# Optimization experiments

Measured on AMD Instinct MI355X. Metric: run time of the kernel, lower is better.

The kernel has to match this reference:

```python
import jax, jax.numpy as jnp
import numpy as np

NEG_INF = -1e9

def setup_inputs() -> dict:
    key = jax.random.key(0)
    ks = jax.random.split(key, 7)
    B, NQ, NK, DQ, DK, DV, DH = 16, 128, 2048, 256, 256, 128, 64
    queries = jax.random.normal(ks[0], (B, NQ, DQ), dtype=jnp.float32)
    keys = jax.random.normal(ks[1], (B, NK, DK), dtype=jnp.float32)
    values = jax.random.normal(ks[2], (B, NK, DV), dtype=jnp.float32)
    valid_lens = jax.random.randint(ks[3], (B,), 1, NK + 1, dtype=jnp.int32)
    Wq = jax.random.normal(ks[4], (DQ, DH), dtype=jnp.float32) / np.sqrt(DQ)
    Wk = jax.random.normal(ks[5], (DK, DH), dtype=jnp.float32) / np.sqrt(DK)
    wv = jax.random.normal(ks[6], (DH,), dtype=jnp.float32) / np.sqrt(DH)
    return {"queries": queries, "keys": keys, "values": values,
            "valid_lens": valid_lens, "Wq": Wq, "Wk": Wk, "wv": wv}


def reference(queries, keys, values, valid_lens, Wq, Wk, wv):
    # Additive (Bahdanau) attention.
    q = jnp.einsum('bqd,dh->bqh', queries, Wq)   # [B, nq, dH]
    k = jnp.einsum('bkd,dh->bkh', keys, Wk)      # [B, nk, dH]
    # broadcast add -> tanh -> reduce with wv: scores [B, nq, nk]
    feat = jnp.tanh(q[:, :, None, :] + k[:, None, :, :])  # [B, nq, nk, dH]
    scores = jnp.einsum('bqkh,h->bqk', feat, wv)
    # masked softmax over nk using per-batch valid lengths
    nk = keys.shape[1]
    mask = jnp.arange(nk)[None, None, :] < valid_lens[:, None, None]  # [B,1,nk]
    scores = jnp.where(mask, scores, NEG_INF)
    attn = jax.nn.softmax(scores, axis=-1)
    # dropout is identity at eval time
    return jnp.einsum('bqk,bkv->bqv', attn, values)  # [B, nq, dv]
```

## Files before the change

### kernel.cpp

```cpp
#include <hip/hip_runtime.h>
#include <stddef.h>


__device__ __forceinline__ float fast_rcp(float x)  { return __builtin_amdgcn_rcpf(x); }
__device__ __forceinline__ float fast_exp2(float x) { return __builtin_amdgcn_exp2f(x); }

#define C2F 2.88539008177792681f
#define L2E 1.44269504088896340f

template<int MODE>
__device__ __forceinline__
void proj_body(const float* __restrict__ inb, const float* __restrict__ W,
               float* __restrict__ out, int b, int r0, int rowsPerB, int t)
{
  __shared__ float4 Wlds[256 * 16];
  __shared__ float  klds[64 * 36];

  const float4* W4 = (const float4*)W;
  #pragma unroll
  for (int i = 0; i < 16; ++i) Wlds[t + 256 * i] = W4[t + 256 * i];

  const int j = t >> 4;
  const int g = t & 15;

  float acc[4][4];
  #pragma unroll
  for (int m = 0; m < 4; ++m)
    acc[m][0] = acc[m][1] = acc[m][2] = acc[m][3] = 0.f;

  for (int dc = 0; dc < 8; ++dc) {
    {
      const int row = t >> 2, cs = (t & 3) * 8;
      const float* s = inb + row * 256 + dc * 32 + cs;
      float4 a0 = *(const float4*)s;
      float4 a1 = *(const float4*)(s + 4);
      float* dst = &klds[row * 36 + cs];
      *(float4*)dst       = a0;
      *(float4*)(dst + 4) = a1;
    }
    __syncthreads();
    #pragma unroll
    for (int d = 0; d < 32; ++d) {
      float4 w4 = Wlds[(dc * 32 + d) * 16 + j];
      #pragma unroll
      for (int m = 0; m < 4; ++m) {
        float kv = klds[(g + 16 * m) * 36 + d];
        acc[m][0] = fmaf(kv, w4.x, acc[m][0]);
        acc[m][1] = fmaf(kv, w4.y, acc[m][1]);
        acc[m][2] = fmaf(kv, w4.z, acc[m][2]);
        acc[m][3] = fmaf(kv, w4.w, acc[m][3]);
      }
    }
    __syncthreads();
  }

  if constexpr (MODE == 1) {
    #pragma unroll
    for (int m = 0; m < 4; ++m) {
      int k = r0 + g + 16 * m;
      size_t base = ((size_t)(b * 16 + (k >> 7)) * 64) * 128 + (k & 127);
      #pragma unroll
      for (int i = 0; i < 4; ++i)
        out[base + (size_t)(4 * j + i) * 128] = fast_exp2(C2F * acc[m][i]);
    }
  } else if constexpr (MODE == 2) {
    #pragma unroll
    for (int m = 0; m < 4; ++m) {
      int k = r0 + g + 16 * m;
      size_t base = (size_t)(b * 16 + (k >> 7)) * 8192 + (size_t)(k & 127) * 2;
      float e0 = fast_exp2(C2F * acc[m][0]);
      float e1 = fast_exp2(C2F * acc[m][1]);
      float e2 = fast_exp2(C2F * acc[m][2]);
      float e3 = fast_exp2(C2F * acc[m][3]);
      *(float2*)&out[base + (size_t)(2 * j) * 256]     = make_float2(e0, e1);
      *(float2*)&out[base + (size_t)(2 * j + 1) * 256] = make_float2(e2, e3);
    }
  } else {
    #pragma unroll
    for (int m = 0; m < 4; ++m) {
      int row = r0 + g + 16 * m;
      float4 o;
      o.x = fast_exp2(C2F * acc[m][0]);
      o.y = fast_exp2(C2F * acc[m][1]);
      o.z = fast_exp2(C2F * acc[m][2]);
      o.w = fast_exp2(C2F * acc[m][3]);
      *(float4*)&out[((size_t)b * rowsPerB + row) * 64 + 4 * j] = o;
    }
  }
}

__global__ __launch_bounds__(256)
void proj_qk_kernel(const float* __restrict__ queries, const float* __restrict__ keys,
                    const float* __restrict__ Wq, const float* __restrict__ Wk,
                    float* __restrict__ Eq, float* __restrict__ EkP,
                    const int* __restrict__ vlens)
{
  const int blk = blockIdx.x;
  if (blk >= 512) {
    const int idx = blk - 512;
    const int b = idx & 15, rt = idx >> 4, r0 = rt * 64;
    proj_body<0>(queries + ((size_t)b * 128 + r0) * 256, Wq, Eq, b, r0, 128,
                 threadIdx.x);
  } else {
    const int b = blk & 15, rt = blk >> 4, r0 = rt * 64;
    if (r0 >= vlens[b]) return;
    proj_body<2>(keys + ((size_t)b * 2048 + r0) * 256, Wk, EkP, b, r0, 2048,
                 threadIdx.x);
  }
}

template<int MODE, bool CHECK>
__global__ __launch_bounds__(256)
void proj_kernel(const float* __restrict__ in, const float* __restrict__ W,
                 float* __restrict__ out, const int* __restrict__ vlens,
                 int rowsPerB)
{
  const int t  = threadIdx.x;
  const int b  = blockIdx.x & 15;
  const int rt = blockIdx.x >> 4;
  const int r0 = rt * 64;
  if constexpr (CHECK) {
    if (r0 >= vlens[b]) return;
  }
  proj_body<MODE>(in + ((size_t)b * rowsPerB + r0) * 256, W, out, b, r0,
                  rowsPerB, t);
}

__global__ __launch_bounds__(512, 6)
void scorepv_kernel(const float* __restrict__ Eq, const float* __restrict__ EkP,
                    const float* __restrict__ values, const int* __restrict__ vlens,
                    const float* __restrict__ wv,
                    float* __restrict__ partial, float* __restrict__ tsum)
{
  const int blk = blockIdx.x;
  const int g   = blk >> 3;
  const int qq  = blk & 7;
  const int kt  = g >> 4;
  const int b   = g & 15;
  const int vl  = vlens[b];
  if (kt * 128 >= vl) return;

  __shared__ float ek_lds[64 * 128];

  const int t = threadIdx.x;

  {
    const float4* src = (const float4*)(EkP + (size_t)(b * 16 + kt) * 8192);
    float4* dst = (float4*)ek_lds;
    #pragma unroll
    for (int i = 0; i < 4; ++i) dst[t + 512 * i] = src[t + 512 * i];
  }

  float w0 = 0.f, W1 = 0.f;
  #pragma unroll
  for (int u = 0; u < 16; ++u) {
    float4 v = ((const float4*)wv)[u];
    w0 += v.x + v.y + v.z + v.w;
    W1 += fabsf(v.x) + fabsf(v.y) + fabsf(v.z) + fabsf(v.w);
  }

  __syncthreads();

  const int wave_u = __builtin_amdgcn_readfirstlane(t >> 6);
  const int lane   = t & 63;
  const int q0g    = qq * 16 + wave_u * 2;
  const int kp     = lane * 2;
  const float* eqb = Eq + (size_t)(b * 128 + q0g) * 64;

  float s[2][2] = {{w0, w0}, {w0, w0}};

  const float4* ek4 = (const float4*)ek_lds;
  #pragma unroll 8
  for (int hp = 0; hp < 32; ++hp) {
    float4 e = ek4[hp * 64 + lane];
    float2 wvp = *(const float2*)&wv[2 * hp];
    float wa = -2.0f * wvp.x, wb = -2.0f * wvp.y;
    #pragma unroll
    for (int q = 0; q < 2; ++q) {
      float2 eqp = *(const float2*)&eqb[q * 64 + 2 * hp];
      { float x0 = fmaf(eqp.x, e.x, 1.f), x1 = fmaf(eqp.y, e.y, 1.f);
        float y = fast_rcp(x0 * x1);
        float a = wb * x0; a = fmaf(wa, x1, a);
        s[q][0] = fmaf(a, y, s[q][0]); }
      { float x0 = fmaf(eqp.x, e.z, 1.f), x1 = fmaf(eqp.y, e.w, 1.f);
        float y = fast_rcp(x0 * x1);
        float a = wb * x0; a = fmaf(wa, x1, a);
        s[q][1] = fmaf(a, y, s[q][1]); }
    }
  }

  const int kbase = kt * 128 + kp;
  float p[2][2];
  #pragma unroll
  for (int q = 0; q < 2; ++q) {
    p[q][0] = (kbase     < vl) ? fast_exp2((s[q][0] - W1) * L2E) : 0.f;
    p[q][1] = (kbase + 1 < vl) ? fast_exp2((s[q][1] - W1) * L2E) : 0.f;
  }

  #pragma unroll
  for (int q = 0; q < 2; ++q) {
    float e = p[q][0] + p[q][1];
    #pragma unroll
    for (int m = 1; m < 64; m <<= 1) e += __shfl_xor(e, m, 64);
    if (lane == 0) tsum[(size_t)(b * 16 + kt) * 128 + q0g + q] = e;
  }

  __syncthreads();
  float* p_lds = ek_lds;
  const int q0l = wave_u * 2;
  *(float2*)&p_lds[kp * 20 + q0l]       = make_float2(p[0][0], p[1][0]);
  *(float2*)&p_lds[(kp + 1) * 20 + q0l] = make_float2(p[0][1], p[1][1]);
  __syncthreads();

  const int kg = t >> 7, v = t & 127;
  const int kloc = min(128, vl - kt * 128);
  const int k0 = kg * 32, k1 = min(k0 + 32, kloc);
  const int len = (k1 > k0) ? (k1 - k0) : 0;
  const int nfull = len & ~7;
  const float* vb = values + ((size_t)(b * 2048 + kt * 128)) * 128 + v;
  float acc[16];
  #pragma unroll
  for (int i = 0; i < 16; ++i) acc[i] = 0.f;

  for (int kb = k0; kb < k0 + nfull; kb += 8) {
    float vv[8];
    #pragma unroll
    for (int j = 0; j < 8; ++j) vv[j] = vb[(size_t)(kb + j) * 128];
    #pragma unroll
    for (int j = 0; j < 8; ++j) {
      const float* pr = &p_lds[(kb + j) * 20];
      float4 p0 = *(const float4*)&pr[0];
      float4 p1 = *(const float4*)&pr[4];
      float4 p2 = *(const float4*)&pr[8];
      float4 p3 = *(const float4*)&pr[12];
      float vx = vv[j];
      acc[ 0]=fmaf(p0.x,vx,acc[ 0]); acc[ 1]=fmaf(p0.y,vx,acc[ 1]);
      acc[ 2]=fmaf(p0.z,vx,acc[ 2]); acc[ 3]=fmaf(p0.w,vx,acc[ 3]);
      acc[ 4]=fmaf(p1.x,vx,acc[ 4]); acc[ 5]=fmaf(p1.y,vx,acc[ 5]);
      acc[ 6]=fmaf(p1.z,vx,acc[ 6]); acc[ 7]=fmaf(p1.w,vx,acc[ 7]);
      acc[ 8]=fmaf(p2.x,vx,acc[ 8]); acc[ 9]=fmaf(p2.y,vx,acc[ 9]);
      acc[10]=fmaf(p2.z,vx,acc[10]); acc[11]=fmaf(p2.w,vx,acc[11]);
      acc[12]=fmaf(p3.x,vx,acc[12]); acc[13]=fmaf(p3.y,vx,acc[13]);
      acc[14]=fmaf(p3.z,vx,acc[14]); acc[15]=fmaf(p3.w,vx,acc[15]);
    }
  }
  for (int k = k0 + nfull; k < k1; ++k) {
    float vx = vb[(size_t)k * 128];
    const float* pr = &p_lds[k * 20];
    #pragma unroll
    for (int q = 0; q < 16; ++q) acc[q] = fmaf(pr[q], vx, acc[q]);
  }

  __syncthreads();
  float* red = ek_lds;
  if (kg > 0) {
    #pragma unroll
    for (int q = 0; q < 16; ++q) red[(kg - 1) * 2048 + q * 128 + v] = acc[q];
  }
  __syncthreads();
  if (kg == 0) {
    #pragma unroll
    for (int q = 0; q < 16; ++q) {
      float tot = acc[q] + red[q * 128 + v] + red[2048 + q * 128 + v]
                + red[4096 + q * 128 + v];
      partial[(((size_t)(b * 128 + qq * 16 + q)) * 16 + kt) * 128 + v] = tot;
    }
  }
}

__global__ __launch_bounds__(256)
void reduce_kernel(const float* __restrict__ partial, const float* __restrict__ tsum,
                   const int* __restrict__ vlens, float* __restrict__ out)
{
  const int blk = blockIdx.x;
  const int b   = blk >> 6;
  const int q   = (blk & 63) * 2 + (threadIdx.x >> 7);
  const int v   = threadIdx.x & 127;
  const int ntk = (vlens[b] + 127) >> 7;

  float tot = 0.f;
  for (int i = 0; i < ntk; ++i)
    tot += tsum[(size_t)(b * 16 + i) * 128 + q];

  float acc = 0.f;
  const float* pp = partial + ((size_t)(b * 128 + q)) * 16 * 128 + v;
  for (int i = 0; i < ntk; ++i)
    acc += pp[(size_t)i * 128];

  out[((size_t)(b * 128 + q)) * 128 + v] = acc / tot;
}

__global__ __launch_bounds__(256)
void attn_kernel(const float* __restrict__ Eq, const float* __restrict__ EkT,
                 const float* __restrict__ values, const int* __restrict__ vlens,
                 const float* __restrict__ wv, float* __restrict__ out)
{
  const int t    = threadIdx.x;
  const int b    = blockIdx.x & 15;
  const int qt   = blockIdx.x >> 4;
  const int wave = t >> 6;
  const int lane = t & 63;

  __shared__ float4 sc4[512 * 4];
  __shared__ float  pvp[128 * 5];
  __shared__ float  linvs[4];

  const int vl = vlens[b];

  float eqv[64], wv2[64];
  float w0 = 0.f;
  {
    const float4* eq4 = (const float4*)(Eq + (size_t)(b * 128 + qt * 4 + wave) * 64);
    const float4* wv4 = (const float4*)wv;
    #pragma unroll
    for (int u = 0; u < 16; ++u) {
      float4 e = eq4[u], v = wv4[u];
      eqv[4*u+0] = e.x; eqv[4*u+1] = e.y; eqv[4*u+2] = e.z; eqv[4*u+3] = e.w;
      wv2[4*u+0] = -2.f * v.x; wv2[4*u+1] = -2.f * v.y;
      wv2[4*u+2] = -2.f * v.z; wv2[4*u+3] = -2.f * v.w;
      w0 += v.x + v.y + v.z + v.w;
    }
  }

  const int ktiles = (vl + 127) >> 7;
  const int kp = 2 * lane;
  for (int kt = 0; kt < ktiles; ++kt) {
    const float* tb = EkT + ((size_t)(b * 16 + kt) * 64) * 128 + kp;
    float s0 = w0, s1 = w0;
    #pragma unroll
    for (int h = 0; h < 64; ++h) {
      float2 ek = *(const float2*)(tb + (size_t)h * 128);
      float r0 = fast_rcp(fmaf(eqv[h], ek.x, 1.0f));
      float r1 = fast_rcp(fmaf(eqv[h], ek.y, 1.0f));
      s0 = fmaf(wv2[h], r0, s0);
      s1 = fmaf(wv2[h], r1, s1);
    }
    int k = kt * 128 + kp;
    if (k     >= vl) s0 = -1e9f;
    if (k + 1 >= vl) s1 = -1e9f;
    float* scf = (float*)sc4;
    *(float2*)(scf + (((k >> 2) * 4 + wave) * 4 + (k & 3))) = make_float2(s0, s1);
  }

  const int nq4 = (vl + 3) >> 2;
  float mx = -3e38f;
  for (int Q = lane; Q < nq4; Q += 64) {
    float4 f = sc4[Q * 4 + wave];
    mx = fmaxf(mx, fmaxf(fmaxf(f.x, f.y), fmaxf(f.z, f.w)));
  }
  #pragma unroll
  for (int msk = 1; msk < 64; msk <<= 1) mx = fmaxf(mx, __shfl_xor(mx, msk, 64));
  float lsum = 0.f;
  for (int Q = lane; Q < nq4; Q += 64) {
    float4 f = sc4[Q * 4 + wave];
    f.x = fast_exp2((f.x - mx) * L2E);
    f.y = fast_exp2((f.y - mx) * L2E);
    f.z = fast_exp2((f.z - mx) * L2E);
    f.w = fast_exp2((f.w - mx) * L2E);
    sc4[Q * 4 + wave] = f;
    lsum += f.x + f.y + f.z + f.w;
  }
  #pragma unroll
  for (int msk = 1; msk < 64; msk <<= 1) lsum += __shfl_xor(lsum, msk, 64);
  if (lane == 0) linvs[wave] = fast_rcp(lsum);
  __syncthreads();

  const int grp = t >> 7, v = t & 127;
  float acc[4] = {0.f, 0.f, 0.f, 0.f};
  const float* vb = values + (size_t)b * 2048 * 128 + v;
  for (int Q = grp; Q < nq4; Q += 2) {
    float4 p0 = sc4[Q * 4 + 0], p1 = sc4[Q * 4 + 1];
    float4 p2 = sc4[Q * 4 + 2], p3 = sc4[Q * 4 + 3];
    const float* vk = vb + (size_t)(Q * 4) * 128;
    float x;
    x = vk[0];
    acc[0]=fmaf(p0.x,x,acc[0]); acc[1]=fmaf(p1.x,x,acc[1]);
    acc[2]=fmaf(p2.x,x,acc[2]); acc[3]=fmaf(p3.x,x,acc[3]);
    x = vk[128];
    acc[0]=fmaf(p0.y,x,acc[0]); acc[1]=fmaf(p1.y,x,acc[1]);
    acc[2]=fmaf(p2.y,x,acc[2]); acc[3]=fmaf(p3.y,x,acc[3]);
    x = vk[256];
    acc[0]=fmaf(p0.z,x,acc[0]); acc[1]=fmaf(p1.z,x,acc[1]);
    acc[2]=fmaf(p2.z,x,acc[2]); acc[3]=fmaf(p3.z,x,acc[3]);
    x = vk[384];
    acc[0]=fmaf(p0.w,x,acc[0]); acc[1]=fmaf(p1.w,x,acc[1]);
    acc[2]=fmaf(p2.w,x,acc[2]); acc[3]=fmaf(p3.w,x,acc[3]);
  }
  if (grp == 1) {
    #pragma unroll
    for (int qq = 0; qq < 4; ++qq) pvp[v * 5 + qq] = acc[qq];
  }
  __syncthreads();
  if (grp == 0) {
    #pragma unroll
    for (int qq = 0; qq < 4; ++qq) {
      float tot = acc[qq] + pvp[v * 5 + qq];
      out[((size_t)(b * 128) + qt * 4 + qq) * 128 + v] = tot * linvs[qq];
    }
  }
}

extern "C" void kernel_launch(void* const* d_in, const int* in_sizes, int n_in,
                              void* d_out, int out_size, void* d_ws, size_t ws_size,
                              hipStream_t stream) {
  const float* queries = (const float*)d_in[0];
  const float* keys    = (const float*)d_in[1];
  const float* values  = (const float*)d_in[2];
  const int*   vlens   = (const int*)d_in[3];
  const float* Wq      = (const float*)d_in[4];
  const float* Wk      = (const float*)d_in[5];
  const float* wv      = (const float*)d_in[6];
  float* outp = (float*)d_out;

  float* base    = (float*)d_ws;
  float* Eq      = base;
  float* EkP     = base + 131072;
  float* tsumb   = base + 2228224;
  float* partial = base + 2260992;
  const size_t need = (size_t)(2260992 + 4194304) * 4;

  if (ws_size >= need) {
    hipLaunchKernelGGL(proj_qk_kernel, dim3(544), dim3(256), 0, stream,
                       queries, keys, Wq, Wk, Eq, EkP, vlens);
    hipLaunchKernelGGL(scorepv_kernel, dim3(2048), dim3(512), 0, stream,
                       Eq, EkP, values, vlens, wv, partial, tsumb);
    hipLaunchKernelGGL(reduce_kernel, dim3(1024), dim3(256), 0, stream,
                       partial, tsumb, vlens, outp);
  } else {
    hipLaunchKernelGGL((proj_kernel<0, false>), dim3(32), dim3(256), 0, stream,
                       queries, Wq, Eq, (const int*)nullptr, 128);
    hipLaunchKernelGGL((proj_kernel<1, true>), dim3(512), dim3(256), 0, stream,
                       keys, Wk, EkP, vlens, 2048);
    hipLaunchKernelGGL(attn_kernel, dim3(512), dim3(256), 0, stream,
                       Eq, EkP, values, vlens, wv, outp);
  }
}
```

Baseline: 91.24 us.

## Make score-PV kernel persistent with atomic work queue over 64-key tiles

The score/PV kernel becomes persistent: a fixed grid of 768 blocks pulls work units from a global atomic counter. A small init kernel builds a prefix table over valid 64-key tiles per batch, so only live tiles are scheduled and no blocks launch just to exit early. Key tiles shrink from 128 to 64, with each lane handling one key and two queries. Query and wv values are broadcast via readlane instead of global loads. This aims to balance load across the uneven valid lengths, at the cost of an extra launch, atomic serialization, more partials for the reduce kernel to sum, and a larger workspace.

```diff
diff --git a/kernel.cpp b/kernel.cpp
--- a/kernel.cpp
+++ b/kernel.cpp
@@ -4,9 +4,30 @@
 
 __device__ __forceinline__ float fast_rcp(float x)  { return __builtin_amdgcn_rcpf(x); }
 __device__ __forceinline__ float fast_exp2(float x) { return __builtin_amdgcn_exp2f(x); }
+__device__ __forceinline__ float rlane(float v, int l) {
+  return __int_as_float(__builtin_amdgcn_readlane(__float_as_int(v), l));
+}
 
 #define C2F 2.88539008177792681f
 #define L2E 1.44269504088896340f
+
+#define M_CNTS 0
+#define M_NS   1
+#define M_P64  8
+
+__global__ void init_kernel(const int* __restrict__ vlens, int* __restrict__ meta)
+{
+  if (threadIdx.x == 0) {
+    int as = 0;
+    meta[M_P64] = 0;
+    for (int b = 0; b < 16; ++b) {
+      as += (vlens[b] + 63) >> 6;
+      meta[M_P64 + 1 + b] = as;
+    }
+    meta[M_NS]   = as * 8;
+    meta[M_CNTS] = 0;
+  }
+}
 
 template<int MODE>
 __device__ __forceinline__
@@ -67,13 +88,13 @@
     #pragma unroll
     for (int m = 0; m < 4; ++m) {
       int k = r0 + g + 16 * m;
-      size_t base = (size_t)(b * 16 + (k >> 7)) * 8192 + (size_t)(k & 127) * 2;
+      size_t base = (size_t)(b * 32 + (k >> 6)) * 4096 + (size_t)(k & 63) * 2;
       float e0 = fast_exp2(C2F * acc[m][0]);
       float e1 = fast_exp2(C2F * acc[m][1]);
       float e2 = fast_exp2(C2F * acc[m][2]);
       float e3 = fast_exp2(C2F * acc[m][3]);
-      *(float2*)&out[base + (size_t)(2 * j) * 256]     = make_float2(e0, e1);
-      *(float2*)&out[base + (size_t)(2 * j + 1) * 256] = make_float2(e2, e3);
+      *(float2*)&out[base + (size_t)(2 * j) * 128]     = make_float2(e0, e1);
+      *(float2*)&out[base + (size_t)(2 * j + 1) * 128] = make_float2(e2, e3);
     }
   } else {
     #pragma unroll
@@ -130,28 +151,25 @@
 void scorepv_kernel(const float* __restrict__ Eq, const float* __restrict__ EkP,
                     const float* __restrict__ values, const int* __restrict__ vlens,
                     const float* __restrict__ wv,
-                    float* __restrict__ partial, float* __restrict__ tsum)
-{
-  const int blk = blockIdx.x;
-  const int g   = blk >> 3;
-  const int qq  = blk & 7;
-  const int kt  = g >> 4;
-  const int b   = g & 15;
-  const int vl  = vlens[b];
-  if (kt * 128 >= vl) return;
-
-  __shared__ float ek_lds[64 * 128];
+                    float* __restrict__ partial, float* __restrict__ tsum,
+                    int* __restrict__ meta)
+{
+  __shared__ float ek_lds[4096];
+  __shared__ float p_lds[64 * 20];
+  __shared__ int sh_u, sh_pre[17];
 
   const int t = threadIdx.x;
-
-  {
-    const float4* src = (const float4*)(EkP + (size_t)(b * 16 + kt) * 8192);
-    float4* dst = (float4*)ek_lds;
-    #pragma unroll
-    for (int i = 0; i < 4; ++i) dst[t + 512 * i] = src[t + 512 * i];
-  }
-
-  float w0 = 0.f, W1 = 0.f;
+  if (t < 17) sh_pre[t] = meta[M_P64 + t];
+  const int nunits = meta[M_NS];
+
+  const int wave_u = __builtin_amdgcn_readfirstlane(t >> 6);
+  const int lane   = t & 63;
+  const int q0l    = wave_u * 2;
+
+  float2 wvr = *(const float2*)&wv[2 * (lane & 31)];
+  wvr.x *= -2.0f; wvr.y *= -2.0f;
+
+  float W1 = 0.f, w0 = 0.f;
   #pragma unroll
   for (int u = 0; u < 16; ++u) {
     float4 v = ((const float4*)wv)[u];
@@ -159,111 +177,122 @@
     W1 += fabsf(v.x) + fabsf(v.y) + fabsf(v.z) + fabsf(v.w);
   }
 
-  __syncthreads();
-
-  const int wave_u = __builtin_amdgcn_readfirstlane(t >> 6);
-  const int lane   = t & 63;
-  const int q0g    = qq * 16 + wave_u * 2;
-  const int kp     = lane * 2;
-  const float* eqb = Eq + (size_t)(b * 128 + q0g) * 64;
-
-  float s[2][2] = {{w0, w0}, {w0, w0}};
-
-  const float4* ek4 = (const float4*)ek_lds;
-  #pragma unroll 8
-  for (int hp = 0; hp < 32; ++hp) {
-    float4 e = ek4[hp * 64 + lane];
-    float2 wvp = *(const float2*)&wv[2 * hp];
-    float wa = -2.0f * wvp.x, wb = -2.0f * wvp.y;
-    #pragma unroll
-    for (int q = 0; q < 2; ++q) {
-      float2 eqp = *(const float2*)&eqb[q * 64 + 2 * hp];
-      { float x0 = fmaf(eqp.x, e.x, 1.f), x1 = fmaf(eqp.y, e.y, 1.f);
+  for (;;) {
+    __syncthreads();
+    if (t == 0) sh_u = atomicAdd(&meta[M_CNTS], 1);
+    __syncthreads();
+    const int u = sh_u;
+    if (u >= nunits) break;
+
+    const int w  = u >> 3;
+    const int qq = u & 7;
+    int b = 0;
+    while (w >= sh_pre[1 + b]) ++b;
+    const int kt = w - sh_pre[b];
+    const int vl = vlens[b];
+    const int q0g = qq * 16 + q0l;
+
+    float2 eqr = *(const float2*)&Eq[
+        ((size_t)(b * 128 + q0g + (lane >> 5))) * 64 + 2 * (lane & 31)];
+
+    {
+      const float4* src = (const float4*)(EkP + (size_t)(b * 32 + kt) * 4096);
+      float4* dst = (float4*)ek_lds;
+      dst[t]       = src[t];
+      dst[t + 512] = src[t + 512];
+    }
+    __syncthreads();
+
+    float s0 = w0, s1 = w0;
+    #pragma unroll
+    for (int hp = 0; hp < 32; ++hp) {
+      float2 e = *(const float2*)&ek_lds[hp * 128 + lane * 2];
+      float wa = rlane(wvr.x, hp);
+      float wb = rlane(wvr.y, hp);
+      {
+        float eq0 = rlane(eqr.x, hp);
+        float eq1 = rlane(eqr.y, hp);
+        float x0 = fmaf(eq0, e.x, 1.f), x1 = fmaf(eq1, e.y, 1.f);
         float y = fast_rcp(x0 * x1);
         float a = wb * x0; a = fmaf(wa, x1, a);
-        s[q][0] = fmaf(a, y, s[q][0]); }
-      { float x0 = fmaf(eqp.x, e.z, 1.f), x1 = fmaf(eqp.y, e.w, 1.f);
+        s0 = fmaf(a, y, s0);
+      }
+      {
+        float eq0 = rlane(eqr.x, 32 + hp);
+        float eq1 = rlane(eqr.y, 32 + hp);
+        float x0 = fmaf(eq0, e.x, 1.f), x1 = fmaf(eq1, e.y, 1.f);
         float y = fast_rcp(x0 * x1);
         float a = wb * x0; a = fmaf(wa, x1, a);
-        s[q][1] = fmaf(a, y, s[q][1]); }
-    }
-  }
-
-  const int kbase = kt * 128 + kp;
-  float p[2][2];
-  #pragma unroll
-  for (int q = 0; q < 2; ++q) {
-    p[q][0] = (kbase     < vl) ? fast_exp2((s[q][0] - W1) * L2E) : 0.f;
-    p[q][1] = (kbase + 1 < vl) ? fast_exp2((s[q][1] - W1) * L2E) : 0.f;
-  }
-
-  #pragma unroll
-  for (int q = 0; q < 2; ++q) {
-    float e = p[q][0] + p[q][1];
-    #pragma unroll
-    for (int m = 1; m < 64; m <<= 1) e += __shfl_xor(e, m, 64);
-    if (lane == 0) tsum[(size_t)(b * 16 + kt) * 128 + q0g + q] = e;
-  }
-
-  __syncthreads();
-  float* p_lds = ek_lds;
-  const int q0l = wave_u * 2;
-  *(float2*)&p_lds[kp * 20 + q0l]       = make_float2(p[0][0], p[1][0]);
-  *(float2*)&p_lds[(kp + 1) * 20 + q0l] = make_float2(p[0][1], p[1][1]);
-  __syncthreads();
-
-  const int kg = t >> 7, v = t & 127;
-  const int kloc = min(128, vl - kt * 128);
-  const int k0 = kg * 32, k1 = min(k0 + 32, kloc);
-  const int len = (k1 > k0) ? (k1 - k0) : 0;
-  const int nfull = len & ~7;
-  const float* vb = values + ((size_t)(b * 2048 + kt * 128)) * 128 + v;
-  float acc[16];
-  #pragma unroll
-  for (int i = 0; i < 16; ++i) acc[i] = 0.f;
-
-  for (int kb = k0; kb < k0 + nfull; kb += 8) {
-    float vv[8];
-    #pragma unroll
-    for (int j = 0; j < 8; ++j) vv[j] = vb[(size_t)(kb + j) * 128];
-    #pragma unroll
-    for (int j = 0; j < 8; ++j) {
-      const float* pr = &p_lds[(kb + j) * 20];
-      float4 p0 = *(const float4*)&pr[0];
-      float4 p1 = *(const float4*)&pr[4];
-      float4 p2 = *(const float4*)&pr[8];
-      float4 p3 = *(const float4*)&pr[12];
-      float vx = vv[j];
-      acc[ 0]=fmaf(p0.x,vx,acc[ 0]); acc[ 1]=fmaf(p0.y,vx,acc[ 1]);
-      acc[ 2]=fmaf(p0.z,vx,acc[ 2]); acc[ 3]=fmaf(p0.w,vx,acc[ 3]);
-      acc[ 4]=fmaf(p1.x,vx,acc[ 4]); acc[ 5]=fmaf(p1.y,vx,acc[ 5]);
-      acc[ 6]=fmaf(p1.z,vx,acc[ 6]); acc[ 7]=fmaf(p1.w,vx,acc[ 7]);
-      acc[ 8]=fmaf(p2.x,vx,acc[ 8]); acc[ 9]=fmaf(p2.y,vx,acc[ 9]);
-      acc[10]=fmaf(p2.z,vx,acc[10]); acc[11]=fmaf(p2.w,vx,acc[11]);
-      acc[12]=fmaf(p3.x,vx,acc[12]); acc[13]=fmaf(p3.y,vx,acc[13]);
-      acc[14]=fmaf(p3.z,vx,acc[14]); acc[15]=fmaf(p3.w,vx,acc[15]);
-    }
-  }
-  for (int k = k0 + nfull; k < k1; ++k) {
-    float vx = vb[(size_t)k * 128];
-    const float* pr = &p_lds[k * 20];
-    #pragma unroll
-    for (int q = 0; q < 16; ++q) acc[q] = fmaf(pr[q], vx, acc[q]);
-  }
-
-  __syncthreads();
-  float* red = ek_lds;
-  if (kg > 0) {
-    #pragma unroll
-    for (int q = 0; q < 16; ++q) red[(kg - 1) * 2048 + q * 128 + v] = acc[q];
-  }
-  __syncthreads();
-  if (kg == 0) {
-    #pragma unroll
-    for (int q = 0; q < 16; ++q) {
-      float tot = acc[q] + red[q * 128 + v] + red[2048 + q * 128 + v]
-                + red[4096 + q * 128 + v];
-      partial[(((size_t)(b * 128 + qq * 16 + q)) * 16 + kt) * 128 + v] = tot;
+        s1 = fmaf(a, y, s1);
+      }
+    }
+
+    const int kbase = kt * 64 + lane;
+    float p0 = (kbase < vl) ? fast_exp2((s0 - W1) * L2E) : 0.f;
+    float p1 = (kbase < vl) ? fast_exp2((s1 - W1) * L2E) : 0.f;
+
+    {
+      float e0 = p0, e1 = p1;
+      #pragma unroll
+      for (int m = 1; m < 64; m <<= 1) {
+        e0 += __shfl_xor(e0, m, 64);
+        e1 += __shfl_xor(e1, m, 64);
+      }
+      if (lane == 0) {
+        tsum[(size_t)(b * 32 + kt) * 128 + q0g]     = e0;
+        tsum[(size_t)(b * 32 + kt) * 128 + q0g + 1] = e1;
+      }
+    }
+
+    *(float2*)&p_lds[lane * 20 + q0l] = make_float2(p0, p1);
+    __syncthreads();
+
+    const int qh = t >> 8, kg = (t >> 7) & 1, v = t & 127;
+    const int kloc = min(64, vl - kt * 64);
+    const int k0 = kg * 32, k1 = min(k0 + 32, kloc);
+    const int len = (k1 > k0) ? (k1 - k0) : 0;
+    const int nfull = len & ~7;
+    const float* vb = values + ((size_t)(b * 2048 + kt * 64)) * 128 + v;
+    float acc[8];
+    #pragma unroll
+    for (int i = 0; i < 8; ++i) acc[i] = 0.f;
+
+    for (int kb = k0; kb < k0 + nfull; kb += 8) {
+      float vv[8];
+      #pragma unroll
+      for (int j = 0; j < 8; ++j) vv[j] = vb[(size_t)(kb + j) * 128];
+      #pragma unroll
+      for (int j = 0; j < 8; ++j) {
+        const float* pr = &p_lds[(kb + j) * 20 + qh * 8];
+        float4 pa = *(const float4*)&pr[0];
+        float4 pb = *(const float4*)&pr[4];
+        float vx = vv[j];
+        acc[0]=fmaf(pa.x,vx,acc[0]); acc[1]=fmaf(pa.y,vx,acc[1]);
+        acc[2]=fmaf(pa.z,vx,acc[2]); acc[3]=fmaf(pa.w,vx,acc[3]);
+        acc[4]=fmaf(pb.x,vx,acc[4]); acc[5]=fmaf(pb.y,vx,acc[5]);
+        acc[6]=fmaf(pb.z,vx,acc[6]); acc[7]=fmaf(pb.w,vx,acc[7]);
+      }
+    }
+    for (int k = k0 + nfull; k < k1; ++k) {
+      float vx = vb[(size_t)k * 128];
+      const float* pr = &p_lds[k * 20 + qh * 8];
+      #pragma unroll
+      for (int i = 0; i < 8; ++i) acc[i] = fmaf(pr[i], vx, acc[i]);
+    }
+
+    float* red = ek_lds;
+    if (kg == 1) {
+      #pragma unroll
+      for (int i = 0; i < 8; ++i) red[(qh * 8 + i) * 128 + v] = acc[i];
+    }
+    __syncthreads();
+    if (kg == 0) {
+      #pragma unroll
+      for (int i = 0; i < 8; ++i) {
+        float tot = acc[i] + red[(qh * 8 + i) * 128 + v];
+        partial[(((size_t)(b * 128 + qq * 16 + qh * 8 + i)) * 32 + kt) * 128 + v]
+            = tot;
+      }
     }
   }
 }
@@ -276,14 +305,14 @@
   const int b   = blk >> 6;
   const int q   = (blk & 63) * 2 + (threadIdx.x >> 7);
   const int v   = threadIdx.x & 127;
-  const int ntk = (vlens[b] + 127) >> 7;
+  const int ntk = (vlens[b] + 63) >> 6;
 
   float tot = 0.f;
   for (int i = 0; i < ntk; ++i)
-    tot += tsum[(size_t)(b * 16 + i) * 128 + q];
+    tot += tsum[(size_t)(b * 32 + i) * 128 + q];
 
   float acc = 0.f;
-  const float* pp = partial + ((size_t)(b * 128 + q)) * 16 * 128 + v;
+  const float* pp = partial + ((size_t)(b * 128 + q)) * 32 * 128 + v;
   for (int i = 0; i < ntk; ++i)
     acc += pp[(size_t)i * 128];
 
@@ -416,14 +445,16 @@
   float* Eq      = base;
   float* EkP     = base + 131072;
   float* tsumb   = base + 2228224;
-  float* partial = base + 2260992;
-  const size_t need = (size_t)(2260992 + 4194304) * 4;
+  float* partial = base + 2293760;
+  int*   meta    = (int*)(base + 10682368);
+  const size_t need = (size_t)10682368 * 4 + 256;
 
   if (ws_size >= need) {
+    hipLaunchKernelGGL(init_kernel, dim3(1), dim3(64), 0, stream, vlens, meta);
     hipLaunchKernelGGL(proj_qk_kernel, dim3(544), dim3(256), 0, stream,
                        queries, keys, Wq, Wk, Eq, EkP, vlens);
-    hipLaunchKernelGGL(scorepv_kernel, dim3(2048), dim3(512), 0, stream,
-                       Eq, EkP, values, vlens, wv, partial, tsumb);
+    hipLaunchKernelGGL(scorepv_kernel, dim3(768), dim3(512), 0, stream,
+                       Eq, EkP, values, vlens, wv, partial, tsumb, meta);
     hipLaunchKernelGGL(reduce_kernel, dim3(1024), dim3(256), 0, stream,
                        partial, tsumb, vlens, outp);
   } else {
```

After: 102.5 us. 12.4% more time.
